# Kernel tuning notes

Hardware: AMD Instinct MI355X
Metric: run time of the kernel (lower is better)

The kernel has to match this reference:

```python
import jax, jax.numpy as jnp
import numpy as np

N = 100000   # num_nodes
E = 1000000  # num_edges
H = 64       # h_dim
OUT = 16     # out_dim (num classes)
R = 90       # num_rels
B = 8        # num_bases


def setup_inputs() -> dict:
    key = jax.random.key(0)
    ks = jax.random.split(key, 16)
    feats = jax.random.normal(ks[0], (N, H), dtype=jnp.float32)
    src = jax.random.randint(ks[1], (E,), 0, N)
    dst = jax.random.randint(ks[2], (E,), 0, N)
    etype = jax.random.randint(ks[3], (E,), 0, R)
    norm = jax.random.uniform(ks[4], (E, 1), dtype=jnp.float32)
    s_in = 1.0 / np.sqrt(H)
    s_b = 1.0 / np.sqrt(B)
    # layer 0: H->H, layer 1 (hidden): H->H, layer 2: H->OUT
    coeff0 = jax.random.normal(ks[5], (R, B), dtype=jnp.float32) * s_b
    bases0 = jax.random.normal(ks[6], (B, H, H), dtype=jnp.float32) * s_in
    bias0 = jnp.zeros((H,), dtype=jnp.float32)
    coeff1 = jax.random.normal(ks[7], (R, B), dtype=jnp.float32) * s_b
    bases1 = jax.random.normal(ks[8], (B, H, H), dtype=jnp.float32) * s_in
    bias1 = jnp.zeros((H,), dtype=jnp.float32)
    coeff2 = jax.random.normal(ks[9], (R, B), dtype=jnp.float32) * s_b
    bases2 = jax.random.normal(ks[10], (B, H, OUT), dtype=jnp.float32) * s_in
    bias2 = jnp.zeros((OUT,), dtype=jnp.float32)
    return {
        "feats": feats,
        "coeff0": coeff0, "bases0": bases0, "bias0": bias0,
        "coeff1": coeff1, "bases1": bases1, "bias1": bias1,
        "coeff2": coeff2, "bases2": bases2, "bias2": bias2,
        "src": src, "dst": dst, "etype": etype, "norm": norm,
    }


def _rgcn_layer(x, coeff, bases, bias, src, dst, etype, norm, relu):
    # Basis decomposition: W_r = sum_b coeff[r,b] * bases[b]
    # Project all nodes through every basis once: [N, B, out]
    Hn = jnp.einsum('ni,bio->nbo', x, bases)
    c = coeff[etype]  # [E, B] per-edge basis coefficients
    # Per-edge message m_e = (sum_b c_eb * Hn[src_e, b]) * norm_e,
    # accumulated over the (small, fixed) basis dim to avoid an [E,B,out] buffer.
    m = c[:, 0:1] * Hn[src, 0]
    for b in range(1, bases.shape[0]):
        m = m + c[:, b:b + 1] * Hn[src, b]
    m = m * norm
    h = jax.ops.segment_sum(m, dst, num_segments=x.shape[0]) + bias
    return jax.nn.relu(h) if relu else h


def reference(feats, coeff0, bases0, bias0, coeff1, bases1, bias1,
              coeff2, bases2, bias2, src, dst, etype, norm):
    h = _rgcn_layer(feats, coeff0, bases0, bias0, src, dst, etype, norm, relu=True)
    h = _rgcn_layer(h, coeff1, bases1, bias1, src, dst, etype, norm, relu=True)
    h = _rgcn_layer(h, coeff2, bases2, bias2, src, dst, etype, norm, relu=False)
    return h
```

## Files before the change

### kernel.cpp

```cpp
#include <hip/hip_runtime.h>
#include <hip/hip_bf16.h>
#include <cstdint>

#define NNODES 100000
#define NEDGES 1000000
#define HDIM 64
#define ODIM 16
#define NB 8
#define NREL 90
#define KDIM (HDIM * NB)
#define CPAD 16
#define NRANGE 8
#define RANGE ((NNODES + NRANGE - 1) / NRANGE)

typedef short short8 __attribute__((ext_vector_type(8)));
typedef float f32x4  __attribute__((ext_vector_type(4)));
union FragU { uint4 u; short8 s; };

__device__ __forceinline__ float asf(uint32_t u) { float f; __builtin_memcpy(&f, &u, 4); return f; }
__device__ __forceinline__ uint32_t asu(float f) { uint32_t u; __builtin_memcpy(&u, &f, 4); return u; }
__device__ __forceinline__ uint16_t f2bf(float f) {
    uint32_t x = asu(f);
    return (uint16_t)((x + 0x7FFFu + ((x >> 16) & 1u)) >> 16);
}
__device__ __forceinline__ uint32_t pack2(float lo, float hi) {
    return (uint32_t)f2bf(lo) | ((uint32_t)f2bf(hi) << 16);
}
__device__ __forceinline__ void fmaC(const float4& cA, const float4& cB, float xs,
                                     float* __restrict__ acc) {
    acc[0] = fmaf(cA.x, xs, acc[0]); acc[1] = fmaf(cA.y, xs, acc[1]);
    acc[2] = fmaf(cA.z, xs, acc[2]); acc[3] = fmaf(cA.w, xs, acc[3]);
    acc[4] = fmaf(cB.x, xs, acc[4]); acc[5] = fmaf(cB.y, xs, acc[5]);
    acc[6] = fmaf(cB.z, xs, acc[6]); acc[7] = fmaf(cB.w, xs, acc[7]);
}

__global__ void cast_kernel(const float* __restrict__ in, uint16_t* __restrict__ out, int n4) {
    const int stride = (int)(gridDim.x * blockDim.x);
    for (int idx = (int)(blockIdx.x * blockDim.x + threadIdx.x); idx < n4; idx += stride) {
        float4 v = reinterpret_cast<const float4*>(in)[idx];
        uint2 p;
        p.x = pack2(v.x, v.y);
        p.y = pack2(v.z, v.w);
        reinterpret_cast<uint2*>(out)[idx] = p;
    }
}

__global__ void zero_kernel(int* __restrict__ p, int n) {
    for (int i = (int)(blockIdx.x * blockDim.x + threadIdx.x); i < n;
         i += (int)(gridDim.x * blockDim.x)) p[i] = 0;
}

__global__ void hist_kernel(const int* __restrict__ dst, int* __restrict__ cnt, int nE) {
    const int r     = (int)blockIdx.x & (NRANGE - 1);
    const int chunk = (int)blockIdx.x >> 3;
    const int nchk  = (int)gridDim.x >> 3;
    const int CH    = (nE + nchk - 1) / nchk;
    const int lo    = r * RANGE;
    const int hi    = (lo + RANGE < NNODES) ? lo + RANGE : NNODES;
    const int e1    = ((chunk + 1) * CH < nE) ? (chunk + 1) * CH : nE;
    for (int e = chunk * CH + (int)threadIdx.x; e < e1; e += 256) {
        const int d = dst[e];
        if (d >= lo && d < hi) atomicAdd(&cnt[d * CPAD], 1);
    }
}

#define SCAN_B 512
__launch_bounds__(SCAN_B)
__global__ void scan_partial_kernel(const int* __restrict__ cnt, int* __restrict__ bsum, int n) {
    __shared__ int sh[SCAN_B];
    int id = (int)(blockIdx.x * SCAN_B + threadIdx.x);
    sh[threadIdx.x] = (id < n) ? cnt[id * CPAD] : 0;
    __syncthreads();
    for (int off = SCAN_B / 2; off > 0; off >>= 1) {
        if ((int)threadIdx.x < off) sh[threadIdx.x] += sh[threadIdx.x + off];
        __syncthreads();
    }
    if (threadIdx.x == 0) bsum[blockIdx.x] = sh[0];
}

__launch_bounds__(256)
__global__ void scan_base_kernel(const int* __restrict__ bsum, int* __restrict__ bbase,
                                 int* __restrict__ offs, int nblk, int nNodes) {
    __shared__ int sh[256];
    const int t = (int)threadIdx.x;
    int v = (t < nblk) ? bsum[t] : 0;
    sh[t] = v;
    __syncthreads();
    for (int off = 1; off < 256; off <<= 1) {
        int tmp = (t >= off) ? sh[t - off] : 0;
        __syncthreads();
        sh[t] += tmp;
        __syncthreads();
    }
    if (t < nblk) bbase[t] = sh[t] - v;
    if (t == 255) offs[nNodes] = sh[255];
}

__launch_bounds__(SCAN_B)
__global__ void scan_final_kernel(int* __restrict__ cnt, const int* __restrict__ bbase,
                                  int* __restrict__ offs, int n) {
    __shared__ int sh[SCAN_B];
    int id = (int)(blockIdx.x * SCAN_B + threadIdx.x);
    int v = (id < n) ? cnt[id * CPAD] : 0;
    sh[threadIdx.x] = v;
    __syncthreads();
    for (int off = 1; off < SCAN_B; off <<= 1) {
        int tmp = ((int)threadIdx.x >= off) ? sh[threadIdx.x - off] : 0;
        __syncthreads();
        sh[threadIdx.x] += tmp;
        __syncthreads();
    }
    if (id < n) {
        int excl = sh[threadIdx.x] - v + bbase[blockIdx.x];
        offs[id] = excl;
        cnt[id * CPAD] = excl;
    }
}

__global__ void scatter_kernel(const int* __restrict__ src, const int* __restrict__ dst,
                               const int* __restrict__ et, const float* __restrict__ norm,
                               int* __restrict__ cursor, uint2* __restrict__ rec, int nE) {
    const int r     = (int)blockIdx.x & (NRANGE - 1);
    const int chunk = (int)blockIdx.x >> 3;
    const int nchk  = (int)gridDim.x >> 3;
    const int CH    = (nE + nchk - 1) / nchk;
    const int lo    = r * RANGE;
    const int hi    = (lo + RANGE < NNODES) ? lo + RANGE : NNODES;
    const int e1    = ((chunk + 1) * CH < nE) ? (chunk + 1) * CH : nE;
    for (int e = chunk * CH + (int)threadIdx.x; e < e1; e += 256) {
        const int d = dst[e];
        if (d >= lo && d < hi) {
            int p = atomicAdd(&cursor[d * CPAD], 1);
            rec[p] = make_uint2((uint32_t)src[e] | ((uint32_t)et[e] << 20), asu(norm[e]));
        }
    }
}

__launch_bounds__(256)
__global__ void csr_agg_kernel(const uint16_t* __restrict__ x,
                               const float* __restrict__ coeff,
                               const int* __restrict__ offs,
                               const uint2* __restrict__ rec,
                               uint16_t* __restrict__ G, int nNodes) {
    __shared__ __align__(16) float cS[NREL * NB];
    for (int i = (int)threadIdx.x; i < NREL * NB; i += 256) cS[i] = coeff[i];
    __syncthreads();

    const int hl   = (int)threadIdx.x & 31;
    const int hwid = (int)((blockIdx.x * blockDim.x + threadIdx.x) >> 5);
    const int nhw  = (int)((gridDim.x * blockDim.x) >> 5);

    for (int d = hwid; d < nNodes; d += nhw) {
        const int j0 = offs[d], j1 = offs[d + 1];
        float accL[NB] = {0.f, 0.f, 0.f, 0.f, 0.f, 0.f, 0.f, 0.f};
        float accH[NB] = {0.f, 0.f, 0.f, 0.f, 0.f, 0.f, 0.f, 0.f};
        int j = j0;
        for (; j + 8 <= j1; j += 8) {
            uint2 r[8];
#pragma unroll
            for (int u = 0; u < 8; u++) r[u] = rec[j + u];
            uint32_t w[8];
#pragma unroll
            for (int u = 0; u < 8; u++)
                w[u] = *reinterpret_cast<const uint32_t*>(
                    x + (size_t)(r[u].x & 0xFFFFFu) * HDIM + 2 * hl);
#pragma unroll
            for (int u = 0; u < 8; u++) {
                const float4 cA = *reinterpret_cast<const float4*>(cS + (r[u].x >> 20) * NB);
                const float4 cB = *reinterpret_cast<const float4*>(cS + (r[u].x >> 20) * NB + 4);
                const float nm = asf(r[u].y);
                fmaC(cA, cB, asf(w[u] << 16) * nm, accL);
                fmaC(cA, cB, asf(w[u] & 0xFFFF0000u) * nm, accH);
            }
        }
        for (; j < j1; j++) {
            const uint2 r0 = rec[j];
            const uint32_t w0 = *reinterpret_cast<const uint32_t*>(
                x + (size_t)(r0.x & 0xFFFFFu) * HDIM + 2 * hl);
            const float4 cA = *reinterpret_cast<const float4*>(cS + (r0.x >> 20) * NB);
            const float4 cB = *reinterpret_cast<const float4*>(cS + (r0.x >> 20) * NB + 4);
            const float nm = asf(r0.y);
            fmaC(cA, cB, asf(w0 << 16) * nm, accL);
            fmaC(cA, cB, asf(w0 & 0xFFFF0000u) * nm, accH);
        }
        uint4 lo, hi;
        lo.x = pack2(accL[0], accL[1]); lo.y = pack2(accL[2], accL[3]);
        lo.z = pack2(accL[4], accL[5]); lo.w = pack2(accL[6], accL[7]);
        hi.x = pack2(accH[0], accH[1]); hi.y = pack2(accH[2], accH[3]);
        hi.z = pack2(accH[4], accH[5]); hi.w = pack2(accH[6], accH[7]);
        uint16_t* gp = G + (size_t)d * KDIM + hl * 16;
        *reinterpret_cast<uint4*>(gp)     = lo;
        *reinterpret_cast<uint4*>(gp + 8) = hi;
    }
}

__launch_bounds__(256, 2)
__global__ void proj_hidden_kernel(const uint16_t* __restrict__ G,
                                   const float* __restrict__ bases,
                                   const float* __restrict__ bias,
                                   uint16_t* __restrict__ xout, int nNodes) {
    __shared__ __align__(16) uint4 Gs4[64 * 64];

    const int t    = (int)threadIdx.x;
    const int lane = t & 63;
    const int ot   = t >> 6;
    const int q    = lane >> 4;
    const int c    = lane & 15;

    FragU bf[16];
#pragma unroll
    for (int kb = 0; kb < 16; kb++) {
#pragma unroll
        for (int j = 0; j < 8; j++) {
            const int k = kb * 32 + q * 8 + j;
            const int i = k >> 3, b = k & 7;
            bf[kb].s[j] = (short)f2bf(bases[(size_t)(b * HDIM + i) * HDIM + ot * 16 + c]);
        }
    }
    const float bv = bias[ot * 16 + c];

    const int nTiles = (nNodes + 63) / 64;
    for (int tile = (int)blockIdx.x; tile < nTiles; tile += (int)gridDim.x) {
        for (int idx = t; idx < 64 * 64; idx += 256) {
            const int row = idx >> 6, g = idx & 63;
            int arow = tile * 64 + row;
            if (arow > nNodes - 1) arow = nNodes - 1;
            Gs4[(row << 6) | (g ^ (row & 7))] =
                *reinterpret_cast<const uint4*>(G + (size_t)arow * KDIM + g * 8);
        }
        __syncthreads();

#pragma unroll
        for (int g = 0; g < 4; g++) {
            const int row = g * 16 + c;
            f32x4 acc = {0.f, 0.f, 0.f, 0.f};
#pragma unroll
            for (int kb = 0; kb < 16; kb++) {
                FragU a;
                a.u = Gs4[(row << 6) | ((kb * 4 + q) ^ (row & 7))];
                acc = __builtin_amdgcn_mfma_f32_16x16x32_bf16(a.s, bf[kb].s, acc, 0, 0, 0);
            }
            const int nbase = tile * 64 + g * 16 + q * 4;
#pragma unroll
            for (int r = 0; r < 4; r++) {
                const int node = nbase + r;
                if (node < nNodes) {
                    float v = fmaxf(acc[r] + bv, 0.f);
                    xout[(size_t)node * HDIM + ot * 16 + c] = f2bf(v);
                }
            }
        }
        __syncthreads();
    }
}

__launch_bounds__(256, 3)
__global__ void proj_out_kernel(const uint16_t* __restrict__ G,
                                const float* __restrict__ bases,
                                const float* __restrict__ bias,
                                float* __restrict__ out, int nNodes) {
    const int t    = (int)threadIdx.x;
    const int lane = t & 63;
    const int w    = t >> 6;
    const int q    = lane >> 4;
    const int c    = lane & 15;

    FragU bf[16];
#pragma unroll
    for (int kb = 0; kb < 16; kb++) {
#pragma unroll
        for (int j = 0; j < 8; j++) {
            const int k = kb * 32 + q * 8 + j;
            const int i = k >> 3, b = k & 7;
            bf[kb].s[j] = (short)f2bf(bases[(size_t)(b * HDIM + i) * ODIM + c]);
        }
    }
    const float bv = bias[c];

    const int nTiles = (nNodes + 63) / 64;
    for (int tile = (int)blockIdx.x; tile < nTiles; tile += (int)gridDim.x) {
        int arow = tile * 64 + w * 16 + c;
        if (arow > nNodes - 1) arow = nNodes - 1;
        const uint16_t* gp = G + (size_t)arow * KDIM + q * 8;

        f32x4 acc = {0.f, 0.f, 0.f, 0.f};
#pragma unroll
        for (int kb = 0; kb < 16; kb++) {
            FragU a;
            a.u = *reinterpret_cast<const uint4*>(gp + kb * 32);
            acc = __builtin_amdgcn_mfma_f32_16x16x32_bf16(a.s, bf[kb].s, acc, 0, 0, 0);
        }

        const int nbase = tile * 64 + w * 16 + q * 4;
#pragma unroll
        for (int r = 0; r < 4; r++) {
            const int node = nbase + r;
            if (node < nNodes) out[(size_t)node * ODIM + c] = acc[r] + bv;
        }
    }
}

extern "C" void kernel_launch(void* const* d_in, const int* in_sizes, int n_in,
                              void* d_out, int out_size, void* d_ws, size_t ws_size,
                              hipStream_t stream) {
    const float* feats  = (const float*)d_in[0];
    const float* coeff0 = (const float*)d_in[1];
    const float* bases0 = (const float*)d_in[2];
    const float* bias0  = (const float*)d_in[3];
    const float* coeff1 = (const float*)d_in[4];
    const float* bases1 = (const float*)d_in[5];
    const float* bias1  = (const float*)d_in[6];
    const float* coeff2 = (const float*)d_in[7];
    const float* bases2 = (const float*)d_in[8];
    const float* bias2  = (const float*)d_in[9];
    const int*   src    = (const int*)d_in[10];
    const int*   dst    = (const int*)d_in[11];
    const int*   etype  = (const int*)d_in[12];
    const float* norm   = (const float*)d_in[13];
    float* out = (float*)d_out;

    char* base = (char*)d_ws;
    uint16_t* G = (uint16_t*)base;
    int* curs   = (int*)base;
    uint16_t* x = (uint16_t*)(base + (size_t)NNODES * KDIM * 2);
    const size_t OFF_OFFS  = 115200000;
    const size_t OFF_BSUM  = OFF_OFFS + 800032;
    const size_t OFF_BBASE = OFF_BSUM + 1024;
    const size_t OFF_REC   = OFF_BBASE + 1024;
    int*   offs  = (int*)(base + OFF_OFFS);
    int*   bsum  = (int*)(base + OFF_BSUM);
    int*   bbase = (int*)(base + OFF_BBASE);
    uint2* rec   = (uint2*)(base + OFF_REC);

    const int nblk = (NNODES + SCAN_B - 1) / SCAN_B;

    hipLaunchKernelGGL(zero_kernel, dim3(2048), dim3(256), 0, stream, curs, NNODES * CPAD);
    hipLaunchKernelGGL(hist_kernel, dim3(2048), dim3(256), 0, stream, dst, curs, NEDGES);
    hipLaunchKernelGGL(scan_partial_kernel, dim3(nblk), dim3(SCAN_B), 0, stream, curs, bsum, NNODES);
    hipLaunchKernelGGL(scan_base_kernel, dim3(1), dim3(256), 0, stream, bsum, bbase, offs, nblk, NNODES);
    hipLaunchKernelGGL(scan_final_kernel, dim3(nblk), dim3(SCAN_B), 0, stream, curs, bbase, offs, NNODES);
    hipLaunchKernelGGL(scatter_kernel, dim3(2048), dim3(256), 0, stream,
                       src, dst, etype, norm, curs, rec, NEDGES);

    hipLaunchKernelGGL(cast_kernel, dim3(2048), dim3(256), 0, stream,
                       feats, x, NNODES * HDIM / 4);

    hipLaunchKernelGGL(csr_agg_kernel, dim3(2048), dim3(256), 0, stream,
                       x, coeff0, offs, rec, G, NNODES);
    hipLaunchKernelGGL(proj_hidden_kernel, dim3(1024), dim3(256), 0, stream,
                       G, bases0, bias0, x, NNODES);
    hipLaunchKernelGGL(csr_agg_kernel, dim3(2048), dim3(256), 0, stream,
                       x, coeff1, offs, rec, G, NNODES);
    hipLaunchKernelGGL(proj_hidden_kernel, dim3(1024), dim3(256), 0, stream,
                       G, bases1, bias1, x, NNODES);
    hipLaunchKernelGGL(csr_agg_kernel, dim3(2048), dim3(256), 0, stream,
                       x, coeff2, offs, rec, G, NNODES);
    hipLaunchKernelGGL(proj_out_kernel, dim3(1024), dim3(256), 0, stream,
                       G, bases2, bias2, out, NNODES);
}
```

Measured before the change: 428.3 us.

## Sort destination nodes by in-degree before CSR aggregation for load balance

Adds a counting sort of destination nodes by in-degree (descending, degrees above 63 lumped into the first bucket) and has the aggregation kernel walk nodes in that permuted order. Half-wavefronts that share a wave then process nodes with similar edge counts, which cuts divergence and tail imbalance in the edge loop. The cost is four extra small kernel launches, atomics on 64 counters across 100k nodes, and an extra indirection plus less locality in the output writes. The dcnt buffer is placed inside the G region, which is only written later by the first aggregation.

```diff
diff --git a/kernel.cpp b/kernel.cpp
--- a/kernel.cpp
+++ b/kernel.cpp
@@ -136,11 +136,48 @@
     }
 }
 
+__global__ void deg_zero_kernel(int* __restrict__ p) {
+    if (threadIdx.x < 128) p[threadIdx.x] = 0;
+}
+
+__global__ void deg_hist_kernel(const int* __restrict__ offs, int* __restrict__ dcnt, int n) {
+    for (int d = (int)(blockIdx.x * blockDim.x + threadIdx.x); d < n;
+         d += (int)(gridDim.x * blockDim.x)) {
+        int deg = offs[d + 1] - offs[d];
+        int b = (deg > 63) ? 0 : (63 - deg);
+        atomicAdd(&dcnt[b], 1);
+    }
+}
+
+__launch_bounds__(64)
+__global__ void deg_scan_kernel(const int* __restrict__ dcnt, int* __restrict__ dcur) {
+    int t = (int)threadIdx.x;
+    int v = dcnt[t];
+    int s = v;
+    for (int off = 1; off < 64; off <<= 1) {
+        int u = __shfl_up(s, off);
+        if (t >= off) s += u;
+    }
+    dcur[t] = s - v;
+}
+
+__global__ void deg_scatter_kernel(const int* __restrict__ offs, int* __restrict__ dcur,
+                                   int* __restrict__ perm, int n) {
+    for (int d = (int)(blockIdx.x * blockDim.x + threadIdx.x); d < n;
+         d += (int)(gridDim.x * blockDim.x)) {
+        int deg = offs[d + 1] - offs[d];
+        int b = (deg > 63) ? 0 : (63 - deg);
+        int p = atomicAdd(&dcur[b], 1);
+        perm[p] = d;
+    }
+}
+
 __launch_bounds__(256)
 __global__ void csr_agg_kernel(const uint16_t* __restrict__ x,
                                const float* __restrict__ coeff,
                                const int* __restrict__ offs,
                                const uint2* __restrict__ rec,
+                               const int* __restrict__ perm,
                                uint16_t* __restrict__ G, int nNodes) {
     __shared__ __align__(16) float cS[NREL * NB];
     for (int i = (int)threadIdx.x; i < NREL * NB; i += 256) cS[i] = coeff[i];
@@ -150,7 +187,8 @@
     const int hwid = (int)((blockIdx.x * blockDim.x + threadIdx.x) >> 5);
     const int nhw  = (int)((gridDim.x * blockDim.x) >> 5);
 
-    for (int d = hwid; d < nNodes; d += nhw) {
+    for (int i = hwid; i < nNodes; i += nhw) {
+        const int d = perm[i];
         const int j0 = offs[d], j1 = offs[d + 1];
         float accL[NB] = {0.f, 0.f, 0.f, 0.f, 0.f, 0.f, 0.f, 0.f};
         float accH[NB] = {0.f, 0.f, 0.f, 0.f, 0.f, 0.f, 0.f, 0.f};
@@ -322,12 +360,16 @@
     char* base = (char*)d_ws;
     uint16_t* G = (uint16_t*)base;
     int* curs   = (int*)base;
+    int* dcnt   = (int*)(base + 8000000);
+    int* dcur   = dcnt + 64;
     uint16_t* x = (uint16_t*)(base + (size_t)NNODES * KDIM * 2);
     const size_t OFF_OFFS  = 115200000;
+    const size_t OFF_PERM  = OFF_OFFS + 400016;
     const size_t OFF_BSUM  = OFF_OFFS + 800032;
     const size_t OFF_BBASE = OFF_BSUM + 1024;
     const size_t OFF_REC   = OFF_BBASE + 1024;
     int*   offs  = (int*)(base + OFF_OFFS);
+    int*   perm  = (int*)(base + OFF_PERM);
     int*   bsum  = (int*)(base + OFF_BSUM);
     int*   bbase = (int*)(base + OFF_BBASE);
     uint2* rec   = (uint2*)(base + OFF_REC);
@@ -342,19 +384,24 @@
     hipLaunchKernelGGL(scatter_kernel, dim3(2048), dim3(256), 0, stream,
                        src, dst, etype, norm, curs, rec, NEDGES);
 
+    hipLaunchKernelGGL(deg_zero_kernel, dim3(1), dim3(128), 0, stream, dcnt);
+    hipLaunchKernelGGL(deg_hist_kernel, dim3(256), dim3(256), 0, stream, offs, dcnt, NNODES);
+    hipLaunchKernelGGL(deg_scan_kernel, dim3(1), dim3(64), 0, stream, dcnt, dcur);
+    hipLaunchKernelGGL(deg_scatter_kernel, dim3(256), dim3(256), 0, stream, offs, dcur, perm, NNODES);
+
     hipLaunchKernelGGL(cast_kernel, dim3(2048), dim3(256), 0, stream,
                        feats, x, NNODES * HDIM / 4);
 
     hipLaunchKernelGGL(csr_agg_kernel, dim3(2048), dim3(256), 0, stream,
-                       x, coeff0, offs, rec, G, NNODES);
+                       x, coeff0, offs, rec, perm, G, NNODES);
     hipLaunchKernelGGL(proj_hidden_kernel, dim3(1024), dim3(256), 0, stream,
                        G, bases0, bias0, x, NNODES);
     hipLaunchKernelGGL(csr_agg_kernel, dim3(2048), dim3(256), 0, stream,
-                       x, coeff1, offs, rec, G, NNODES);
+                       x, coeff1, offs, rec, perm, G, NNODES);
     hipLaunchKernelGGL(proj_hidden_kernel, dim3(1024), dim3(256), 0, stream,
                        G, bases1, bias1, x, NNODES);
     hipLaunchKernelGGL(csr_agg_kernel, dim3(2048), dim3(256), 0, stream,
-                       x, coeff2, offs, rec, G, NNODES);
+                       x, coeff2, offs, rec, perm, G, NNODES);
     hipLaunchKernelGGL(proj_out_kernel, dim3(1024), dim3(256), 0, stream,
                        G, bases2, bias2, out, NNODES);
 }
```

Result: slower. 1.093 ms (+155.2%).
